# Performance work log

Measured on AMD Instinct MI355X. Metric: run time of the kernel, lower is better.

## Reference

```python
import jax, jax.numpy as jnp
import numpy as np
from jax import lax

N_HEADS = 16
EPS = 1e-6
CHUNK = 128  # chunk size for the causal kv cumsum scan


def causal_dot_product(q, k, v):
    """Equivalent to cumsum over outer-products: out[l] = q[l] . sum_{j<=l} k[j] v[j]^T.
    Chunked lax.scan avoids materializing the [B,H,L,D,M] tensor.
    q,k: [B,H,L,D], v: [B,H,L,M] -> [B,H,L,M]."""
    B, H, L, D = q.shape
    M = v.shape[-1]
    nc = L // CHUNK
    qc = q.reshape(B, H, nc, CHUNK, D).transpose(2, 0, 1, 3, 4)
    kc = k.reshape(B, H, nc, CHUNK, D).transpose(2, 0, 1, 3, 4)
    vc = v.reshape(B, H, nc, CHUNK, M).transpose(2, 0, 1, 3, 4)

    def step(kv_carry, inp):
        qb, kb, vb = inp  # [B,H,C,D], [B,H,C,D], [B,H,C,M]
        kv = jnp.einsum('bhcd,bhcm->bhcdm', kb, vb)
        kv_cum = jnp.cumsum(kv, axis=2) + kv_carry[:, :, None]
        out = jnp.einsum('bhcd,bhcdm->bhcm', qb, kv_cum)
        return kv_cum[:, :, -1], out

    init = jnp.zeros((B, H, D, M), q.dtype)
    _, outs = lax.scan(step, init, (qc, kc, vc))  # outs: [nc,B,H,C,M]
    return outs.transpose(1, 2, 0, 3, 4).reshape(B, H, L, M)


def flow_attention_causal(x, Wq, bq, Wk, bk, Wv, bv, Wo, bo):
    B, L, _ = x.shape
    d_model = Wq.shape[1]
    H = N_HEADS
    # projections -> [B,H,L,D]
    q = (x @ Wq + bq).reshape(B, L, H, -1).transpose(0, 2, 1, 3)
    k = (x @ Wk + bk).reshape(B, L, H, -1).transpose(0, 2, 1, 3)
    v = (x @ Wv + bv).reshape(B, L, H, -1).transpose(0, 2, 1, 3)
    # kernel_method = sigmoid
    q = jax.nn.sigmoid(q)
    k = jax.nn.sigmoid(k)

    sink_incoming = 1.0 / jnp.einsum('bhld,bhld->bhl', q + EPS, jnp.cumsum(k, axis=2) + EPS)
    source_outgoing = 1.0 / jnp.einsum('bhld,bhld->bhl', k + EPS, jnp.cumsum(q, axis=2) + EPS)
    normal = (jnp.arange(L, dtype=x.dtype) + 1.0)[None, None, :]  # [1,1,L]
    sink_incoming = sink_incoming * normal
    source_outgoing = source_outgoing * normal

    conserved_sink = jnp.einsum(
        'bhld,bhld->bhl', q + EPS,
        jnp.cumsum(k * source_outgoing[..., None], axis=2) + EPS) / normal
    conserved_source = jnp.einsum(
        'bhld,bhld->bhl', k + EPS,
        jnp.cumsum(q * sink_incoming[..., None], axis=2) + EPS) / normal

    sink_allocation = jax.nn.sigmoid(conserved_sink)
    cs = jnp.exp(conserved_source)
    source_competition = cs / jnp.cumsum(cs, axis=-1) * normal

    out = causal_dot_product(
        q * (sink_incoming / normal)[..., None],
        k,
        v * source_competition[..., None]) * sink_allocation[..., None]
    out = out.transpose(0, 2, 1, 3).reshape(B, L, d_model)
    return out @ Wo + bo  # dropout is identity at eval


def setup_inputs() -> dict:
    key = jax.random.key(0)
    ks = jax.random.split(key, 9)
    B, L, d_model = 4, 4096, 1024
    s = 0.02
    return {
        'x': jax.random.normal(ks[0], (B, L, d_model), dtype=jnp.float32),
        'Wq': jax.random.normal(ks[1], (d_model, d_model), dtype=jnp.float32) * s,
        'bq': jnp.zeros((d_model,), dtype=jnp.float32),
        'Wk': jax.random.normal(ks[2], (d_model, d_model), dtype=jnp.float32) * s,
        'bk': jnp.zeros((d_model,), dtype=jnp.float32),
        'Wv': jax.random.normal(ks[3], (d_model, d_model), dtype=jnp.float32) * s,
        'bv': jnp.zeros((d_model,), dtype=jnp.float32),
        'Wo': jax.random.normal(ks[4], (d_model, d_model), dtype=jnp.float32) * s,
        'bo': jnp.zeros((d_model,), dtype=jnp.float32),
    }


def reference(x, Wq, bq, Wk, bk, Wv, bv, Wo, bo):
    return flow_attention_causal(x, Wq, bq, Wk, bk, Wv, bv, Wo, bo)
```

## Files before the change

### kernel.cpp

```cpp
#include <hip/hip_runtime.h>
#include <stdint.h>

#define B_ 4
#define L_ 4096
#define DM 1024
#define H_ 16
#define D_ 64
#define BH (B_*H_)
#define N_ (B_*L_)
#define CS 128
#define NC (L_/CS)
#define SC 64
#define NSC (L_/SC)
#define EPSF 1e-6f

typedef unsigned short u16;
typedef unsigned int   u32;
typedef __attribute__((ext_vector_type(8))) short s16x8;
typedef __attribute__((ext_vector_type(4))) float f32x4;

__device__ __forceinline__ float bf2f(u16 u){
  union { u32 i; float f; } v; v.i = ((u32)u) << 16; return v.f;
}
__device__ __forceinline__ u16 f2bf(float f){
  union { float f; u32 i; } v; v.f = f;
  u32 i = v.i;
  return (u16)((i + 0x7fffu + ((i >> 16) & 1u)) >> 16);
}
__device__ __forceinline__ void gload16(const void* g, void* l){
  __builtin_amdgcn_global_load_lds(
      (const __attribute__((address_space(1))) u32*)g,
      (__attribute__((address_space(3))) u32*)l, 16, 0, 0);
}
__device__ __forceinline__ f32x4 mfma16(s16x8 a, s16x8 b, f32x4 c){
  return __builtin_amdgcn_mfma_f32_16x16x32_bf16(a, b, c, 0, 0, 0);
}
__device__ __forceinline__ float sigmoidf_(float x){ return 1.0f/(1.0f+__expf(-x)); }

__global__ void cvt_kernel(const float* __restrict__ in, u16* __restrict__ out, int n4){
  int i = blockIdx.x * blockDim.x + threadIdx.x;
  if (i >= n4) return;
  float4 v = ((const float4*)in)[i];
  union { u16 s[4]; uint2 u; } o;
  o.s[0]=f2bf(v.x); o.s[1]=f2bf(v.y); o.s[2]=f2bf(v.z); o.s[3]=f2bf(v.w);
  ((uint2*)out)[i] = o.u;
}

__global__ __launch_bounds__(256) void transpose_w4_kernel(
    const float* __restrict__ Wq, const float* __restrict__ Wk,
    const float* __restrict__ Wv, const float* __restrict__ Wo,
    u16* __restrict__ wqkvT, u16* __restrict__ woT){
  __shared__ float t[64][65];
  int z = blockIdx.z;
  const float* W = (z==0) ? Wq : (z==1) ? Wk : (z==2) ? Wv : Wo;
  u16* WT = (z<3) ? (wqkvT + (size_t)z*DM*DM) : woT;
  int n0 = blockIdx.x * 64, k0 = blockIdx.y * 64;
  int tx = threadIdx.x & 63, ty = threadIdx.x >> 6;
  #pragma unroll
  for (int s = 0; s < 64; s += 4)
    t[ty + s][tx] = W[(size_t)(k0 + ty + s) * DM + n0 + tx];
  __syncthreads();
  #pragma unroll
  for (int s = 0; s < 64; s += 4)
    WT[(size_t)(n0 + ty + s) * DM + k0 + tx] = f2bf(t[tx][ty + s]);
}

template<int QKV>
__global__ __launch_bounds__(512, 2) void gemm256_kernel(
    const u16* __restrict__ A, const u16* __restrict__ BT,
    const float* __restrict__ biasq, const float* __restrict__ biask, const float* __restrict__ biasv,
    u16* __restrict__ oq, u16* __restrict__ ok, u16* __restrict__ ov,
    float* __restrict__ outf,
    float* __restrict__ sumQ, float* __restrict__ sumK, int NBY)
{
  __shared__ __align__(16) u16 smem[65536];
  char* smb = (char*)smem;
  int tid = threadIdx.x;
  int wave = tid >> 6, lane = tid & 63;
  int wm = wave >> 2, wn = wave & 3;
  int nwg = gridDim.x;
  int q8 = nwg >> 3;
  int id = blockIdx.x;
  int id2 = (id & 7) * q8 + (id >> 3);
  int bx = id2 / NBY, by = id2 % NBY;
  int m0 = bx * 256, n0 = by * 256;
  int srcq = (tid & 7) ^ ((tid >> 3) & 7);
  const u16* aRow = A  + (size_t)(m0 + (tid >> 3)) * 1024 + srcq * 8;
  const u16* bRow = BT + (size_t)(n0 + (tid >> 3)) * 1024 + srcq * 8;

  f32x4 acc[8][4];
  #pragma unroll
  for (int i=0;i<8;i++)
    #pragma unroll
    for (int j=0;j<4;j++) acc[i][j] = (f32x4){0.f,0.f,0.f,0.f};

  int fr = lane & 15, q = lane >> 4;
  int aoff0 = fr*128 + (((q ^ (lane&3)) + 4*((lane>>2)&1)) << 4);
  int aoff1 = fr*128 + (((q ^ (lane&3)) + 4*(1 ^ ((lane>>2)&1))) << 4);

  #define STAGE(s, t) { \
    _Pragma("unroll") \
    for (int i_ = 0; i_ < 4; i_++){ \
      gload16(aRow + (size_t)(t)*64 + (size_t)i_*65536, smb + (s)*32768 + i_*8192 + tid*16); \
      gload16(bRow + (size_t)(t)*64 + (size_t)i_*65536, smb + 65536 + (s)*32768 + i_*8192 + tid*16); \
    } }

  #define COMPUTE(s) { \
    const char* Ab_ = smb + (s)*32768 + wm*16384; \
    const char* Bb_ = smb + 65536 + (s)*32768 + wn*8192; \
    _Pragma("unroll") \
    for (int kk_ = 0; kk_ < 2; kk_++){ \
      int off_ = kk_ ? aoff1 : aoff0; \
      s16x8 af_[8], bf_[4]; \
      _Pragma("unroll") \
      for (int mi_ = 0; mi_ < 8; mi_++) af_[mi_] = *(const s16x8*)(Ab_ + mi_*2048 + off_); \
      _Pragma("unroll") \
      for (int ni_ = 0; ni_ < 4; ni_++) bf_[ni_] = *(const s16x8*)(Bb_ + ni_*2048 + off_); \
      _Pragma("unroll") \
      for (int mi_ = 0; mi_ < 8; mi_++) \
        _Pragma("unroll") \
        for (int ni_ = 0; ni_ < 4; ni_++) \
          acc[mi_][ni_] = mfma16(af_[mi_], bf_[ni_], acc[mi_][ni_]); \
    } }

  STAGE(0, 0)
  STAGE(1, 1)
  for (int t = 0; t < 14; t++){
    asm volatile("s_waitcnt vmcnt(8)" ::: "memory");
    __builtin_amdgcn_s_barrier();
    asm volatile("" ::: "memory");
    COMPUTE(t & 1)
    asm volatile("s_waitcnt lgkmcnt(0)" ::: "memory");
    __builtin_amdgcn_s_barrier();
    asm volatile("" ::: "memory");
    STAGE(t & 1, t + 2)
  }
  asm volatile("s_waitcnt vmcnt(8)" ::: "memory");
  __builtin_amdgcn_s_barrier();
  asm volatile("" ::: "memory");
  COMPUTE(0)
  asm volatile("s_waitcnt vmcnt(0)" ::: "memory");
  __builtin_amdgcn_s_barrier();
  asm volatile("" ::: "memory");
  COMPUTE(1)

  int colblk = n0 + wn*64;
  int which  = QKV ? (colblk >> 10) : 0;
  int cl0    = QKV ? (colblk & 1023) : colblk;
  const float* bias = QKV ? (which==0 ? biasq : (which==1 ? biask : biasv)) : biasq;
  u16* outp = QKV ? (which==0 ? oq : (which==1 ? ok : ov)) : (u16*)0;
  float cs0[4] = {0.f,0.f,0.f,0.f}, cs1[4] = {0.f,0.f,0.f,0.f};
  #pragma unroll
  for (int mi = 0; mi < 8; mi++){
    int row = m0 + wm*128 + mi*16 + (lane>>4)*4;
    #pragma unroll
    for (int ni = 0; ni < 4; ni++){
      int cl = cl0 + ni*16 + fr;
      float bv = bias[cl];
      #pragma unroll
      for (int r = 0; r < 4; r++){
        float val = acc[mi][ni][r] + bv;
        if (QKV){
          if (which < 2) val = sigmoidf_(val);
          outp[(size_t)(row + r) * 1024 + cl] = f2bf(val);
          if (which < 2){ if (mi < 4) cs0[ni] += val; else cs1[ni] += val; }
        } else {
          outf[(size_t)(row + r) * 1024 + cl] = val;
        }
      }
    }
  }
  if (QKV && which < 2){
    float* sums = (which==0) ? sumQ : sumK;
    int bh = (m0 >> 12) * H_ + ((colblk & 1023) >> 6);
    int sc0 = ((m0 & 4095) >> 6) + wm*2;
    #pragma unroll
    for (int h2 = 0; h2 < 2; h2++){
      #pragma unroll
      for (int ni = 0; ni < 4; ni++){
        float s = h2 ? cs1[ni] : cs0[ni];
        s += __shfl_xor(s, 16);
        s += __shfl_xor(s, 32);
        if (lane < 16) sums[((size_t)bh*NSC + sc0 + h2)*64 + ni*16 + fr] = s;
      }
    }
  }
  #undef STAGE
  #undef COMPUTE
}

__global__ __launch_bounds__(64) void scan2_kernel(float* __restrict__ A, float* __restrict__ Bv){
  int bh = blockIdx.x, d = threadIdx.x;
  float ra = 0.f, rb = 0.f;
  for (int g = 0; g < NSC; g += 16){
    float ta[16], tb[16];
    #pragma unroll
    for (int j = 0; j < 16; j++){
      size_t o = ((size_t)bh * NSC + g + j) * 64 + d;
      ta[j] = A[o]; tb[j] = Bv[o];
    }
    #pragma unroll
    for (int j = 0; j < 16; j++){
      size_t o = ((size_t)bh * NSC + g + j) * 64 + d;
      A[o] = ra; Bv[o] = rb;
      ra += ta[j]; rb += tb[j];
    }
  }
}

__global__ __launch_bounds__(64) void siso_fused_kernel(
    const u16* __restrict__ q, const u16* __restrict__ k,
    const float* __restrict__ sumQx, const float* __restrict__ sumKx,
    float* __restrict__ si, float* __restrict__ so,
    float* __restrict__ sumQsi, float* __restrict__ sumKso)
{
  __shared__ u16 cq[64*64];
  __shared__ u16 ck[64*64];
  __shared__ float siv[64], sov[64];
  int bhc = blockIdx.x; int bh = bhc >> 6, sc = bhc & 63;
  int b = bh >> 4, h = bh & 15;
  int lane = threadIdx.x;
  size_t gbase = ((size_t)(b*L_ + sc*SC))*DM + h*D_;
  size_t lb = (size_t)bh*L_ + sc*SC;
  {
    float runQ = sumQx[bhc*64 + lane];
    float runK = sumKx[bhc*64 + lane];
    for (int l = 0; l < SC; l++){
      runQ += bf2f(q[gbase + (size_t)l*DM + lane]);
      runK += bf2f(k[gbase + (size_t)l*DM + lane]);
      int sw = lane ^ (l & 31);
      cq[l*64 + sw] = f2bf(runQ);
      ck[l*64 + sw] = f2bf(runK);
    }
  }
  __syncthreads();
  {
    int l = lane;
    const u16* qrow = q + gbase + (size_t)l*DM;
    const u16* krow = k + gbase + (size_t)l*DM;
    uint4 qr[8], kr[8];
    #pragma unroll
    for (int j=0;j<8;j++){ qr[j]=((const uint4*)qrow)[j]; kr[j]=((const uint4*)krow)[j]; }
    const u16* qp = (const u16*)qr; const u16* kp = (const u16*)kr;
    float a = 0.f, b2 = 0.f;
    #pragma unroll
    for (int d = 0; d < 64; d++){
      int sw = d ^ (l & 31);
      a  += (bf2f(qp[d])+EPSF) * (bf2f(ck[l*64+sw])+EPSF);
      b2 += (bf2f(kp[d])+EPSF) * (bf2f(cq[l*64+sw])+EPSF);
    }
    float n = (float)(sc*SC + l + 1);
    float vsi = n/a, vso = n/b2;
    si[lb+l] = vsi; so[lb+l] = vso;
    siv[l] = vsi;   sov[l] = vso;
    __syncthreads();
    #pragma unroll
    for (int d = 0; d < 64; d++){
      int sw = d ^ (l & 31);
      cq[l*64 + sw] = qp[d];
      ck[l*64 + sw] = kp[d];
    }
  }
  __syncthreads();
  {
    float sq = 0.f, sk = 0.f;
    for (int l = 0; l < SC; l++){
      int sw = lane ^ (l & 31);
      sq += bf2f(cq[l*64 + sw]) * siv[l];
      sk += bf2f(ck[l*64 + sw]) * sov[l];
    }
    sumQsi[bhc*64 + lane] = sq;
    sumKso[bhc*64 + lane] = sk;
  }
}

__global__ __launch_bounds__(64) void cons_fused_kernel(
    const u16* __restrict__ q, const u16* __restrict__ k,
    const float* __restrict__ si, const float* __restrict__ so,
    const float* __restrict__ sumQsiX, const float* __restrict__ sumKsoX,
    float* __restrict__ csrc, float* __restrict__ sall, float* __restrict__ csSum)
{
  __shared__ u16 cq[64*64];
  __shared__ u16 ck[64*64];
  __shared__ float siv[64], sov[64];
  int bhc = blockIdx.x; int bh = bhc >> 6, sc = bhc & 63;
  int b = bh >> 4, h = bh & 15;
  int lane = threadIdx.x;
  size_t gbase = ((size_t)(b*L_ + sc*SC))*DM + h*D_;
  size_t lb = (size_t)bh*L_ + sc*SC;
  siv[lane] = si[lb + lane];
  sov[lane] = so[lb + lane];
  __syncthreads();
  {
    float runQ = sumQsiX[bhc*64 + lane];
    float runK = sumKsoX[bhc*64 + lane];
    for (int l = 0; l < SC; l++){
      runQ += bf2f(q[gbase + (size_t)l*DM + lane]) * siv[l];
      runK += bf2f(k[gbase + (size_t)l*DM + lane]) * sov[l];
      int sw = lane ^ (l & 31);
      cq[l*64 + sw] = f2bf(runQ);
      ck[l*64 + sw] = f2bf(runK);
    }
  }
  __syncthreads();
  {
    int l = lane;
    const u16* qrow = q + gbase + (size_t)l*DM;
    const u16* krow = k + gbase + (size_t)l*DM;
    uint4 qr[8], kr[8];
    #pragma unroll
    for (int j=0;j<8;j++){ qr[j]=((const uint4*)qrow)[j]; kr[j]=((const uint4*)krow)[j]; }
    const u16* qp = (const u16*)qr; const u16* kp = (const u16*)kr;
    float a = 0.f, b2 = 0.f;
    #pragma unroll
    for (int d = 0; d < 64; d++){
      int sw = d ^ (l & 31);
      a  += (bf2f(qp[d])+EPSF) * (bf2f(ck[l*64+sw])+EPSF);
      b2 += (bf2f(kp[d])+EPSF) * (bf2f(cq[l*64+sw])+EPSF);
    }
    float inv = 1.0f / (float)(sc*SC + l + 1);
    sall[lb+l] = sigmoidf_(a * inv);
    float cs = b2 * inv;
    csrc[lb+l] = cs;
    float e = __expf(cs);
    #pragma unroll
    for (int off = 32; off > 0; off >>= 1) e += __shfl_xor(e, off);
    if (lane == 0) csSum[bhc] = e;
  }
}

__global__ __launch_bounds__(64) void scomp_kernel(
    const float* __restrict__ csrc, const float* __restrict__ csSum,
    float* __restrict__ scomp){
  int bhc = blockIdx.x; int bh = bhc >> 6, sc = bhc & 63;
  int lane = threadIdx.x;
  float v2 = (lane < sc) ? csSum[bh*NSC + lane] : 0.f;
  #pragma unroll
  for (int o = 32; o > 0; o >>= 1) v2 += __shfl_xor(v2, o);
  float off = v2;
  size_t idx = (size_t)bh * L_ + sc * SC + lane;
  float cs = __expf(csrc[idx]);
  float run = cs;
  #pragma unroll
  for (int o = 1; o < 64; o <<= 1){
    float t = __shfl_up(run, o);
    if (lane >= o) run += t;
  }
  scomp[idx] = cs / (off + run) * (float)(sc*SC + lane + 1);
}

__global__ __launch_bounds__(256) void vk_chunk_kernel(
    const u16* __restrict__ k, const u16* __restrict__ v,
    const float* __restrict__ scomp, float* __restrict__ vkc){
  __shared__ __align__(16) u16 vt[64*128];
  __shared__ __align__(16) u16 kt[64*128];
  int bhc = blockIdx.x; int bh = bhc >> 5, c = bhc & 31;
  int b = bh >> 4, h = bh & 15;
  int tid = threadIdx.x, wave = tid >> 6, lane = tid & 63;
  size_t gbase = ((size_t)(b * L_ + c * CS)) * DM + h * D_;
  size_t sbase = (size_t)bh * L_ + c * CS;
  {
    int r = tid >> 1;
    int cc = (tid & 1) * 32;
    float vscale = scomp[sbase + r];
    #pragma unroll
    for (int j = 0; j < 4; j++){
      uint4 ku = *(const uint4*)(k + gbase + (size_t)r * DM + cc + j*8);
      uint4 vu = *(const uint4*)(v + gbase + (size_t)r * DM + cc + j*8);
      const u16* kp = (const u16*)&ku; const u16* vp = (const u16*)&vu;
      #pragma unroll
      for (int e = 0; e < 8; e++){
        int m = cc + j*8 + e;
        int idx = m*128 + ((((r >> 3) ^ (m & 7)) << 3) | (r & 7));
        vt[idx] = f2bf(bf2f(vp[e]) * vscale);
        kt[idx] = kp[e];
      }
    }
  }
  __syncthreads();
  int fr = lane & 15, q = lane >> 4;
  int mt = wave;
  f32x4 acc[4];
  #pragma unroll
  for (int i = 0; i < 4; i++) acc[i] = (f32x4){0.f,0.f,0.f,0.f};
  #pragma unroll
  for (int ks = 0; ks < 4; ks++){
    int lc = ks*4 + q;
    int off = ((lc ^ (fr & 7)) << 3);
    s16x8 av = *(const s16x8*)&vt[(mt*16 + fr)*128 + off];
    #pragma unroll
    for (int nt = 0; nt < 4; nt++){
      s16x8 bk = *(const s16x8*)&kt[(nt*16 + fr)*128 + off];
      acc[nt] = mfma16(av, bk, acc[nt]);
    }
  }
  float* outp = vkc + (size_t)bhc * (D_*D_);
  #pragma unroll
  for (int nt = 0; nt < 4; nt++)
    #pragma unroll
    for (int r = 0; r < 4; r++)
      outp[(mt*16 + q*4 + r)*64 + nt*16 + fr] = acc[nt][r];
}

__global__ __launch_bounds__(256) void vk_scan_kernel(const float* __restrict__ vkc, u16* __restrict__ vkb){
  int idx = blockIdx.x * 256 + threadIdx.x;
  int bh = idx >> 12;
  int e  = idx & 4095;
  size_t base = ((size_t)bh * NC) * 4096 + e;
  float run = 0.f;
  for (int g = 0; g < NC; g += 16){
    float tv[16];
    #pragma unroll
    for (int j = 0; j < 16; j++) tv[j] = vkc[base + (size_t)(g + j) * 4096];
    #pragma unroll
    for (int j = 0; j < 16; j++){
      vkb[base + (size_t)(g + j) * 4096] = f2bf(run);
      run += tv[j];
    }
  }
}

__global__ __launch_bounds__(256) void attn_kernel(
    const u16* __restrict__ q, const u16* __restrict__ k, const u16* __restrict__ v,
    const float* __restrict__ si, const float* __restrict__ scomp, const float* __restrict__ salloc,
    const u16* __restrict__ vkb, u16* __restrict__ attnout)
{
  __shared__ __align__(16) u16 qs[128*64];
  __shared__ __align__(16) u16 ks2[128*64];
  __shared__ __align__(16) u16 vts[64*128];
  __shared__ __align__(16) u16 vks[64*64];
  __shared__ __align__(16) u16 ss[128*64];
  int bhc = blockIdx.x; int bh = bhc >> 5, c = bhc & 31;
  int b = bh >> 4, h = bh & 15;
  int tid = threadIdx.x, wave = tid >> 6, lane = tid & 63;
  size_t gbase = ((size_t)(b * L_ + c * CS)) * DM + h * D_;
  size_t sbase = (size_t)bh * L_ + c * CS;
  {
    int r = tid >> 1;
    int cc = (tid & 1) * 32;
    int l = c * CS + r;
    float qscale = si[sbase + r] / (float)(l + 1);
    float vscale = scomp[sbase + r];
    #pragma unroll
    for (int j = 0; j < 4; j++){
      int d0 = cc + j*8;
      uint4 qu = *(const uint4*)(q + gbase + (size_t)r * DM + d0);
      uint4 kuv = *(const uint4*)(k + gbase + (size_t)r * DM + d0);
      uint4 vu = *(const uint4*)(v + gbase + (size_t)r * DM + d0);
      const u16* qp = (const u16*)&qu; const u16* vp = (const u16*)&vu;
      u16 tmp[8];
      #pragma unroll
      for (int e = 0; e < 8; e++) tmp[e] = f2bf(bf2f(qp[e]) * qscale);
      int csw = ((d0 >> 3) ^ (r & 7)) << 3;
      *(uint4*)&qs[r*64 + csw]  = *(uint4*)tmp;
      *(uint4*)&ks2[r*64 + csw] = kuv;
      #pragma unroll
      for (int e = 0; e < 8; e++){
        int m = d0 + e;
        int jsw = (((r >> 3) ^ (m & 7)) << 3) | (r & 7);
        vts[m*128 + jsw] = f2bf(bf2f(vp[e]) * vscale);
      }
    }
    const u16* vkp = vkb + (size_t)bhc * (D_*D_) + tid * 16;
    int m = tid >> 2, dq = (tid & 3) * 2;
    int o0 = ((dq     ^ (m & 7)) << 3);
    int o1 = (((dq+1) ^ (m & 7)) << 3);
    *(uint4*)&vks[m*64 + o0] = *(const uint4*)(vkp);
    *(uint4*)&vks[m*64 + o1] = *(const uint4*)(vkp + 8);
  }
  __syncthreads();
  int t0 = wave, t1 = 7 - wave;
  int fr = lane & 15, qh = lane >> 4;
  int f7 = fr & 7;
  f32x4 acc[2][4];
  #pragma unroll
  for (int i=0;i<2;i++)
    #pragma unroll
    for (int j=0;j<4;j++) acc[i][j] = (f32x4){0.f,0.f,0.f,0.f};
  s16x8 aq[2][2];
  #pragma unroll
  for (int ti = 0; ti < 2; ti++){
    int t = ti ? t1 : t0;
    #pragma unroll
    for (int kk = 0; kk < 2; kk++){
      int oc = (((kk*4 + qh) ^ f7) << 3);
      aq[ti][kk] = *(const s16x8*)&qs[(t*16 + fr)*64 + oc];
    }
  }
  #pragma unroll
  for (int mt = 0; mt < 4; mt++){
    #pragma unroll
    for (int kk = 0; kk < 2; kk++){
      int oc = (((kk*4 + qh) ^ f7) << 3);
      s16x8 bv = *(const s16x8*)&vks[(mt*16 + fr)*64 + oc];
      acc[0][mt] = mfma16(aq[0][kk], bv, acc[0][mt]);
      acc[1][mt] = mfma16(aq[1][kk], bv, acc[1][mt]);
    }
  }
  for (int jt2 = 0; jt2 < 2; jt2++){
    __syncthreads();
    #pragma unroll
    for (int ti = 0; ti < 2; ti++){
      int t = ti ? t1 : t0;
      #pragma unroll
      for (int u = 0; u < 4; u++){
        int jj = jt2*4 + u;
        f32x4 sacc = (f32x4){0.f,0.f,0.f,0.f};
        if (jj <= t){
          #pragma unroll
          for (int kk = 0; kk < 2; kk++){
            int oc = (((kk*4 + qh) ^ f7) << 3);
            s16x8 bkf = *(const s16x8*)&ks2[(jj*16 + fr)*64 + oc];
            sacc = mfma16(aq[ti][kk], bkf, sacc);
          }
        }
        int lrow = t*16 + qh*4;
        int jcol = jj*16 + fr;
        int cst = u*2 + (fr >> 3);
        #pragma unroll
        for (int r = 0; r < 4; r++){
          float sv = (jcol <= lrow + r) ? sacc[r] : 0.f;
          int row = lrow + r;
          ss[row*64 + (((cst ^ (row & 7)) << 3) | f7)] = f2bf(sv);
        }
      }
    }
    __syncthreads();
    #pragma unroll
    for (int ti = 0; ti < 2; ti++){
      int t = ti ? t1 : t0;
      #pragma unroll
      for (int ks = 0; ks < 2; ks++){
        if (jt2*64 + ks*32 <= t*16 + 15){
          int ocs = (((ks*4 + qh) ^ f7) << 3);
          s16x8 as = *(const s16x8*)&ss[(t*16 + fr)*64 + ocs];
          #pragma unroll
          for (int mt = 0; mt < 4; mt++){
            int lc = jt2*8 + ks*4 + qh;
            int ocv = ((lc ^ f7) << 3);
            s16x8 bvv = *(const s16x8*)&vts[(mt*16 + fr)*128 + ocv];
            acc[ti][mt] = mfma16(as, bvv, acc[ti][mt]);
          }
        }
      }
    }
  }
  #pragma unroll
  for (int ti = 0; ti < 2; ti++){
    int t = ti ? t1 : t0;
    int lrow = t*16 + qh*4;
    #pragma unroll
    for (int r = 0; r < 4; r++){
      float sa = salloc[sbase + lrow + r];
      size_t orow = ((size_t)(b * L_ + c * CS + lrow + r)) * DM + h * D_;
      #pragma unroll
      for (int mt = 0; mt < 4; mt++){
        attnout[orow + mt*16 + fr] = f2bf(acc[ti][mt][r] * sa);
      }
    }
  }
}

extern "C" void kernel_launch(void* const* d_in, const int* in_sizes, int n_in,
                              void* d_out, int out_size, void* d_ws, size_t ws_size,
                              hipStream_t stream){
  (void)in_sizes; (void)n_in; (void)out_size; (void)ws_size;
  const float* x  = (const float*)d_in[0];
  const float* Wq = (const float*)d_in[1];
  const float* bq = (const float*)d_in[2];
  const float* Wk = (const float*)d_in[3];
  const float* bk = (const float*)d_in[4];
  const float* Wv = (const float*)d_in[5];
  const float* bv = (const float*)d_in[6];
  const float* Wo = (const float*)d_in[7];
  const float* bo = (const float*)d_in[8];

  char* p = (char*)d_ws;
  auto carve = [&](size_t bytes) -> void* {
    void* r = (void*)p; p += (bytes + 255) & ~(size_t)255; return r;
  };
  u16* xb    = (u16*)carve((size_t)N_*DM*2);
  u16* wqkvT = (u16*)carve((size_t)3*DM*DM*2);
  u16* woT   = (u16*)carve((size_t)DM*DM*2);
  u16* qb  = (u16*)carve((size_t)N_*DM*2);
  u16* kb  = (u16*)carve((size_t)N_*DM*2);
  u16* vb  = (u16*)carve((size_t)N_*DM*2);
  u16* ao  = (u16*)carve((size_t)N_*DM*2);
  float* si   = (float*)carve((size_t)BH*L_*4);
  float* so   = (float*)carve((size_t)BH*L_*4);
  float* csrc = (float*)carve((size_t)BH*L_*4);
  float* sall = (float*)carve((size_t)BH*L_*4);
  float* scmp = (float*)carve((size_t)BH*L_*4);
  float* sumQ   = (float*)carve((size_t)BH*NSC*D_*4);
  float* sumK   = (float*)carve((size_t)BH*NSC*D_*4);
  float* sumQsi = (float*)carve((size_t)BH*NSC*D_*4);
  float* sumKso = (float*)carve((size_t)BH*NSC*D_*4);
  float* csSum  = (float*)carve((size_t)BH*NSC*4);
  float* vkc    = (float*)carve((size_t)BH*NC*(size_t)(D_*D_)*4);
  u16*   vkb    = (u16*)carve((size_t)BH*NC*(size_t)(D_*D_)*2);

  cvt_kernel<<<(N_*DM/4 + 255)/256, 256, 0, stream>>>(x, xb, N_*DM/4);
  transpose_w4_kernel<<<dim3(DM/64, DM/64, 4), 256, 0, stream>>>(Wq, Wk, Wv, Wo, wqkvT, woT);
  gemm256_kernel<1><<<dim3((N_/256)*(3*DM/256)), 512, 0, stream>>>(
      xb, wqkvT, bq, bk, bv, qb, kb, vb, nullptr, sumQ, sumK, 3*DM/256);
  scan2_kernel<<<BH, 64, 0, stream>>>(sumQ, sumK);
  siso_fused_kernel<<<BH*NSC, 64, 0, stream>>>(qb, kb, sumQ, sumK, si, so, sumQsi, sumKso);
  scan2_kernel<<<BH, 64, 0, stream>>>(sumQsi, sumKso);
  cons_fused_kernel<<<BH*NSC, 64, 0, stream>>>(qb, kb, si, so, sumQsi, sumKso, csrc, sall, csSum);
  scomp_kernel<<<BH*NSC, 64, 0, stream>>>(csrc, csSum, scmp);
  vk_chunk_kernel<<<BH*NC, 256, 0, stream>>>(kb, vb, scmp, vkc);
  vk_scan_kernel<<<(BH*D_*D_)/256, 256, 0, stream>>>(vkc, vkb);
  attn_kernel<<<BH*NC, 256, 0, stream>>>(qb, kb, vb, si, scmp, sall, vkb, ao);
  gemm256_kernel<0><<<dim3((N_/256)*(DM/256)), 512, 0, stream>>>(
      ao, woT, bo, bo, bo, nullptr, nullptr, nullptr, (float*)d_out, nullptr, nullptr, DM/256);
}
```

Baseline: 332.5 us.

## Split q/k work across two wavefronts and stage tiles via vectorized LDS loads

The siso and cons fused kernels now launch 128 threads, with one wavefront handling the q stream and the other the k stream, where before a single wave did both. The 64x64 bf16 tiles are first loaded with coalesced 16-byte loads into swizzled LDS, and the sequential prefix scans then run from LDS rather than issuing strided 2-byte global loads per row. In siso, the row registers are kept and reused to rewrite the raw tile. The aim is to cut global load latency and double the parallelism in these small latency-bound kernels, at the cost of extra barriers and LDS traffic.

```diff
diff --git a/kernel.cpp b/kernel.cpp
--- a/kernel.cpp
+++ b/kernel.cpp
@@ -208,7 +208,7 @@
   }
 }
 
-__global__ __launch_bounds__(64) void siso_fused_kernel(
+__global__ __launch_bounds__(128) void siso_fused_kernel(
     const u16* __restrict__ q, const u16* __restrict__ k,
     const float* __restrict__ sumQx, const float* __restrict__ sumKx,
     float* __restrict__ si, float* __restrict__ so,
@@ -219,62 +219,74 @@
   __shared__ float siv[64], sov[64];
   int bhc = blockIdx.x; int bh = bhc >> 6, sc = bhc & 63;
   int b = bh >> 4, h = bh & 15;
-  int lane = threadIdx.x;
+  int tid = threadIdx.x, w = tid >> 6, lane = tid & 63;
   size_t gbase = ((size_t)(b*L_ + sc*SC))*DM + h*D_;
   size_t lb = (size_t)bh*L_ + sc*SC;
-  {
-    float runQ = sumQx[bhc*64 + lane];
-    float runK = sumKx[bhc*64 + lane];
+  const u16* src = w ? k : q;
+  u16* ldsT = w ? ck : cq;
+  {
+    int r8 = lane >> 3, c8 = (lane & 7) * 8;
+    #pragma unroll
+    for (int j = 0; j < 8; j++){
+      int l = j*8 + r8;
+      uint4 u = *(const uint4*)(src + gbase + (size_t)l*DM + c8);
+      const u16* up = (const u16*)&u;
+      #pragma unroll
+      for (int e = 0; e < 8; e++)
+        ldsT[l*64 + ((c8 + e) ^ (l & 31))] = up[e];
+    }
+  }
+  __syncthreads();
+  {
+    float run = w ? sumKx[bhc*64 + lane] : sumQx[bhc*64 + lane];
     for (int l = 0; l < SC; l++){
-      runQ += bf2f(q[gbase + (size_t)l*DM + lane]);
-      runK += bf2f(k[gbase + (size_t)l*DM + lane]);
       int sw = lane ^ (l & 31);
-      cq[l*64 + sw] = f2bf(runQ);
-      ck[l*64 + sw] = f2bf(runK);
-    }
-  }
-  __syncthreads();
+      run += bf2f(ldsT[l*64 + sw]);
+      ldsT[l*64 + sw] = f2bf(run);
+    }
+  }
+  __syncthreads();
+  uint4 rowreg[8];
   {
     int l = lane;
-    const u16* qrow = q + gbase + (size_t)l*DM;
-    const u16* krow = k + gbase + (size_t)l*DM;
-    uint4 qr[8], kr[8];
-    #pragma unroll
-    for (int j=0;j<8;j++){ qr[j]=((const uint4*)qrow)[j]; kr[j]=((const uint4*)krow)[j]; }
-    const u16* qp = (const u16*)qr; const u16* kp = (const u16*)kr;
-    float a = 0.f, b2 = 0.f;
+    const u16* row = src + gbase + (size_t)l*DM;
+    #pragma unroll
+    for (int j=0;j<8;j++) rowreg[j] = ((const uint4*)row)[j];
+    const u16* rp = (const u16*)rowreg;
+    const u16* other = w ? cq : ck;
+    float acc = 0.f;
     #pragma unroll
     for (int d = 0; d < 64; d++){
       int sw = d ^ (l & 31);
-      a  += (bf2f(qp[d])+EPSF) * (bf2f(ck[l*64+sw])+EPSF);
-      b2 += (bf2f(kp[d])+EPSF) * (bf2f(cq[l*64+sw])+EPSF);
+      acc += (bf2f(rp[d])+EPSF) * (bf2f(other[l*64+sw])+EPSF);
     }
     float n = (float)(sc*SC + l + 1);
-    float vsi = n/a, vso = n/b2;
-    si[lb+l] = vsi; so[lb+l] = vso;
-    siv[l] = vsi;   sov[l] = vso;
-    __syncthreads();
-    #pragma unroll
-    for (int d = 0; d < 64; d++){
-      int sw = d ^ (l & 31);
-      cq[l*64 + sw] = qp[d];
-      ck[l*64 + sw] = kp[d];
-    }
-  }
-  __syncthreads();
-  {
-    float sq = 0.f, sk = 0.f;
+    float vv = n / acc;
+    if (w == 0){ si[lb+l] = vv; siv[l] = vv; }
+    else       { so[lb+l] = vv; sov[l] = vv; }
+  }
+  __syncthreads();
+  {
+    int l = lane;
+    const u16* rp = (const u16*)rowreg;
+    #pragma unroll
+    for (int d = 0; d < 64; d++)
+      ldsT[l*64 + (d ^ (l & 31))] = rp[d];
+  }
+  __syncthreads();
+  {
+    const float* sv = w ? sov : siv;
+    float s = 0.f;
     for (int l = 0; l < SC; l++){
       int sw = lane ^ (l & 31);
-      sq += bf2f(cq[l*64 + sw]) * siv[l];
-      sk += bf2f(ck[l*64 + sw]) * sov[l];
-    }
-    sumQsi[bhc*64 + lane] = sq;
-    sumKso[bhc*64 + lane] = sk;
-  }
-}
-
-__global__ __launch_bounds__(64) void cons_fused_kernel(
+      s += bf2f(ldsT[l*64 + sw]) * sv[l];
+    }
+    if (w == 0) sumQsi[bhc*64 + lane] = s;
+    else        sumKso[bhc*64 + lane] = s;
+  }
+}
+
+__global__ __launch_bounds__(128) void cons_fused_kernel(
     const u16* __restrict__ q, const u16* __restrict__ k,
     const float* __restrict__ si, const float* __restrict__ so,
     const float* __restrict__ sumQsiX, const float* __restrict__ sumKsoX,
@@ -285,47 +297,61 @@
   __shared__ float siv[64], sov[64];
   int bhc = blockIdx.x; int bh = bhc >> 6, sc = bhc & 63;
   int b = bh >> 4, h = bh & 15;
-  int lane = threadIdx.x;
+  int tid = threadIdx.x, w = tid >> 6, lane = tid & 63;
   size_t gbase = ((size_t)(b*L_ + sc*SC))*DM + h*D_;
   size_t lb = (size_t)bh*L_ + sc*SC;
-  siv[lane] = si[lb + lane];
-  sov[lane] = so[lb + lane];
-  __syncthreads();
-  {
-    float runQ = sumQsiX[bhc*64 + lane];
-    float runK = sumKsoX[bhc*64 + lane];
+  const u16* src = w ? k : q;
+  u16* ldsT = w ? ck : cq;
+  if (w == 0) siv[lane] = si[lb + lane];
+  else        sov[lane] = so[lb + lane];
+  {
+    int r8 = lane >> 3, c8 = (lane & 7) * 8;
+    #pragma unroll
+    for (int j = 0; j < 8; j++){
+      int l = j*8 + r8;
+      uint4 u = *(const uint4*)(src + gbase + (size_t)l*DM + c8);
+      const u16* up = (const u16*)&u;
+      #pragma unroll
+      for (int e = 0; e < 8; e++)
+        ldsT[l*64 + ((c8 + e) ^ (l & 31))] = up[e];
+    }
+  }
+  __syncthreads();
+  {
+    const float* sv = w ? sov : siv;
+    float run = w ? sumKsoX[bhc*64 + lane] : sumQsiX[bhc*64 + lane];
     for (int l = 0; l < SC; l++){
-      runQ += bf2f(q[gbase + (size_t)l*DM + lane]) * siv[l];
-      runK += bf2f(k[gbase + (size_t)l*DM + lane]) * sov[l];
       int sw = lane ^ (l & 31);
-      cq[l*64 + sw] = f2bf(runQ);
-      ck[l*64 + sw] = f2bf(runK);
+      run += bf2f(ldsT[l*64 + sw]) * sv[l];
+      ldsT[l*64 + sw] = f2bf(run);
     }
   }
   __syncthreads();
   {
     int l = lane;
-    const u16* qrow = q + gbase + (size_t)l*DM;
-    const u16* krow = k + gbase + (size_t)l*DM;
-    uint4 qr[8], kr[8];
-    #pragma unroll
-    for (int j=0;j<8;j++){ qr[j]=((const uint4*)qrow)[j]; kr[j]=((const uint4*)krow)[j]; }
-    const u16* qp = (const u16*)qr; const u16* kp = (const u16*)kr;
-    float a = 0.f, b2 = 0.f;
+    const u16* row = src + gbase + (size_t)l*DM;
+    uint4 rr[8];
+    #pragma unroll
+    for (int j=0;j<8;j++) rr[j] = ((const uint4*)row)[j];
+    const u16* rp = (const u16*)rr;
+    const u16* other = w ? cq : ck;
+    float acc = 0.f;
     #pragma unroll
     for (int d = 0; d < 64; d++){
       int sw = d ^ (l & 31);
-      a  += (bf2f(qp[d])+EPSF) * (bf2f(ck[l*64+sw])+EPSF);
-      b2 += (bf2f(kp[d])+EPSF) * (bf2f(cq[l*64+sw])+EPSF);
+      acc += (bf2f(rp[d])+EPSF) * (bf2f(other[l*64+sw])+EPSF);
     }
     float inv = 1.0f / (float)(sc*SC + l + 1);
-    sall[lb+l] = sigmoidf_(a * inv);
-    float cs = b2 * inv;
-    csrc[lb+l] = cs;
-    float e = __expf(cs);
-    #pragma unroll
-    for (int off = 32; off > 0; off >>= 1) e += __shfl_xor(e, off);
-    if (lane == 0) csSum[bhc] = e;
+    if (w == 0){
+      sall[lb+l] = sigmoidf_(acc * inv);
+    } else {
+      float cs = acc * inv;
+      csrc[lb+l] = cs;
+      float e = __expf(cs);
+      #pragma unroll
+      for (int off = 32; off > 0; off >>= 1) e += __shfl_xor(e, off);
+      if (lane == 0) csSum[bhc] = e;
+    }
   }
 }
 
@@ -604,9 +630,9 @@
   gemm256_kernel<1><<<dim3((N_/256)*(3*DM/256)), 512, 0, stream>>>(
       xb, wqkvT, bq, bk, bv, qb, kb, vb, nullptr, sumQ, sumK, 3*DM/256);
   scan2_kernel<<<BH, 64, 0, stream>>>(sumQ, sumK);
-  siso_fused_kernel<<<BH*NSC, 64, 0, stream>>>(qb, kb, sumQ, sumK, si, so, sumQsi, sumKso);
+  siso_fused_kernel<<<BH*NSC, 128, 0, stream>>>(qb, kb, sumQ, sumK, si, so, sumQsi, sumKso);
   scan2_kernel<<<BH, 64, 0, stream>>>(sumQsi, sumKso);
-  cons_fused_kernel<<<BH*NSC, 64, 0, stream>>>(qb, kb, si, so, sumQsi, sumKso, csrc, sall, csSum);
+  cons_fused_kernel<<<BH*NSC, 128, 0, stream>>>(qb, kb, si, so, sumQsi, sumKso, csrc, sall, csSum);
   scomp_kernel<<<BH*NSC, 64, 0, stream>>>(csrc, csSum, scmp);
   vk_chunk_kernel<<<BH*NC, 256, 0, stream>>>(kb, vb, scmp, vkc);
   vk_scan_kernel<<<(BH*D_*D_)/256, 256, 0, stream>>>(vkc, vkb);
```

Result: no change. 327.8 us (-1.4%).
